# Optimization experiments

Measured on AMD Instinct MI355X. Metric: run time of the kernel, lower is better.

## Reference

```python
import jax, jax.numpy as jnp
import numpy as np
import math

B, T, C = 4, 2048, 1024
H = 16
D_FF = 4 * C


def new_gelu(x):
    # tanh-approx GELU, identical to the torch.jit.script version
    return 0.5 * x * (1.0 + jnp.tanh(math.sqrt(2.0 / math.pi) * (x + 0.044715 * x ** 3)))


def layernorm(x, g, b, eps=1e-5):
    mu = jnp.mean(x, axis=-1, keepdims=True)
    var = jnp.var(x, axis=-1, keepdims=True)
    return (x - mu) * jax.lax.rsqrt(var + eps) * g + b


def setup_inputs() -> dict:
    key = jax.random.key(0)
    ks = jax.random.split(key, 8)
    s = 0.02
    return {
        "x": jax.random.normal(ks[0], (B, T, C), dtype=jnp.float32),
        "ln1_g": jnp.ones((C,), jnp.float32),
        "ln1_b": jnp.zeros((C,), jnp.float32),
        "w_qkv": jax.random.normal(ks[1], (C, 3 * C), jnp.float32) * s,
        "b_qkv": jnp.zeros((3 * C,), jnp.float32),
        "w_attnproj": jax.random.normal(ks[2], (C, C), jnp.float32) * s,
        "b_attnproj": jnp.zeros((C,), jnp.float32),
        "ln2_g": jnp.ones((C,), jnp.float32),
        "ln2_b": jnp.zeros((C,), jnp.float32),
        "w_fc": jax.random.normal(ks[3], (C, D_FF), jnp.float32) * s,
        "b_fc": jnp.zeros((D_FF,), jnp.float32),
        "w_proj": jax.random.normal(ks[4], (D_FF, C), jnp.float32) * s,
        "b_proj": jnp.zeros((C,), jnp.float32),
    }


def _block(x, ln1_g, ln1_b, w_qkv, b_qkv, w_attnproj, b_attnproj,
           ln2_g, ln2_b, w_fc, b_fc, w_proj, b_proj):
    # --- self-attention (pre-LN, non-causal, dropout=0) ---
    h = layernorm(x, ln1_g, ln1_b)
    qkv = h @ w_qkv + b_qkv                       # [B,T,3C]
    q, k, v = jnp.split(qkv, 3, axis=-1)
    hd = C // H
    q = q.reshape(B, T, H, hd).transpose(0, 2, 1, 3)  # [B,H,T,hd]
    k = k.reshape(B, T, H, hd).transpose(0, 2, 1, 3)
    v = v.reshape(B, T, H, hd).transpose(0, 2, 1, 3)
    att = jnp.einsum('bhqd,bhkd->bhqk', q, k) * (1.0 / math.sqrt(hd))
    att = jax.nn.softmax(att, axis=-1)
    y = jnp.einsum('bhqk,bhkd->bhqd', att, v)
    y = y.transpose(0, 2, 1, 3).reshape(B, T, C)
    x = x + (y @ w_attnproj + b_attnproj)
    # --- MLP ---
    h = layernorm(x, ln2_g, ln2_b)
    h = new_gelu(h @ w_fc + b_fc)
    x = x + (h @ w_proj + b_proj)
    return x


def reference(x, ln1_g, ln1_b, w_qkv, b_qkv, w_attnproj, b_attnproj,
              ln2_g, ln2_b, w_fc, b_fc, w_proj, b_proj):
    return _block(x, ln1_g, ln1_b, w_qkv, b_qkv, w_attnproj, b_attnproj,
                  ln2_g, ln2_b, w_fc, b_fc, w_proj, b_proj)
```

## Files before the change

### kernel.cpp

```cpp
#include <hip/hip_runtime.h>


typedef __attribute__((ext_vector_type(8))) short short8;
typedef __attribute__((ext_vector_type(4))) float fx4;
typedef __attribute__((ext_vector_type(16))) float fx16;

__device__ __forceinline__ unsigned short f2bf(float f) {
    union { float f; unsigned u; } v; v.f = f;
    unsigned r = v.u + 0x7fffu + ((v.u >> 16) & 1u);
    return (unsigned short)(r >> 16);
}

__device__ __forceinline__ float fexp2(float x) {
#if __has_builtin(__builtin_amdgcn_exp2f)
    return __builtin_amdgcn_exp2f(x);
#else
    return __expf(x * 0.69314718055994531f);
#endif
}

__device__ __forceinline__ unsigned pack_trunc(float lo, float hi) {
    return __builtin_amdgcn_perm(__float_as_uint(hi), __float_as_uint(lo),
                                 0x07060302u);
}

__device__ __forceinline__ void ld_lds16(const void* g, void* l) {
    __builtin_amdgcn_global_load_lds(
        (const __attribute__((address_space(1))) unsigned int*)g,
        (__attribute__((address_space(3))) unsigned int*)l, 16, 0, 0);
}

__global__ __launch_bounds__(256) void transpose_all(
    const float* __restrict__ w0, unsigned short* __restrict__ o0,
    const float* __restrict__ w1, unsigned short* __restrict__ o1,
    const float* __restrict__ w2, unsigned short* __restrict__ o2,
    const float* __restrict__ w3, unsigned short* __restrict__ o3)
{
    __shared__ float tile[32][33];
    int b = blockIdx.x;
    const float* in; unsigned short* out; int R, Cn;
    if (b < 3072)      { in = w0; out = o0; R = 1024; Cn = 3072; }
    else if (b < 4096) { b -= 3072; in = w1; out = o1; R = 1024; Cn = 1024; }
    else if (b < 8192) { b -= 4096; in = w2; out = o2; R = 1024; Cn = 4096; }
    else               { b -= 8192; in = w3; out = o3; R = 4096; Cn = 1024; }
    int tilesX = Cn >> 5;
    int c0 = (b % tilesX) * 32, r0 = (b / tilesX) * 32;
    int tx = threadIdx.x, ty = threadIdx.y;
    for (int i = 0; i < 4; ++i)
        tile[ty + i * 8][tx] = in[(size_t)(r0 + ty + i * 8) * Cn + c0 + tx];
    __syncthreads();
    for (int i = 0; i < 4; ++i)
        out[(size_t)(c0 + ty + i * 8) * R + r0 + tx] = f2bf(tile[tx][ty + i * 8]);
}

__global__ __launch_bounds__(256) void layernorm_bf16(
    const float* __restrict__ x, const float* __restrict__ g,
    const float* __restrict__ bb, unsigned short* __restrict__ out)
{
    const int C = 1024;
    int row = blockIdx.x;
    const float* xr = x + (size_t)row * C;
    float4 v = ((const float4*)xr)[threadIdx.x];
    float s  = v.x + v.y + v.z + v.w;
    float ss = v.x * v.x + v.y * v.y + v.z * v.z + v.w * v.w;
    for (int off = 32; off >= 1; off >>= 1) {
        s  += __shfl_xor(s,  off);
        ss += __shfl_xor(ss, off);
    }
    __shared__ float sbuf[2][4];
    int wave = threadIdx.x >> 6;
    if ((threadIdx.x & 63) == 0) { sbuf[0][wave] = s; sbuf[1][wave] = ss; }
    __syncthreads();
    s  = sbuf[0][0] + sbuf[0][1] + sbuf[0][2] + sbuf[0][3];
    ss = sbuf[1][0] + sbuf[1][1] + sbuf[1][2] + sbuf[1][3];
    float mu   = s * (1.0f / C);
    float var  = ss * (1.0f / C) - mu * mu;
    float rstd = rsqrtf(var + 1e-5f);
    int i = threadIdx.x * 4;
    ushort4 o;
    o.x = f2bf((v.x - mu) * rstd * g[i + 0] + bb[i + 0]);
    o.y = f2bf((v.y - mu) * rstd * g[i + 1] + bb[i + 1]);
    o.z = f2bf((v.z - mu) * rstd * g[i + 2] + bb[i + 2]);
    o.w = f2bf((v.w - mu) * rstd * g[i + 3] + bb[i + 3]);
    ((ushort4*)(out + (size_t)row * C))[threadIdx.x] = o;
}

template <int EPI, bool SWAP>
__global__ __launch_bounds__(256) void gemm_bt(
    const unsigned short* __restrict__ A, const unsigned short* __restrict__ Bt,
    const float* __restrict__ bias, const float* __restrict__ resid,
    void* __restrict__ out0, void* __restrict__ out1, void* __restrict__ out2,
    int M, int N, int K)
{
    __shared__ unsigned short As[128 * 64];
    __shared__ unsigned short Bs[128 * 64];
    const int bm = (SWAP ? blockIdx.x : blockIdx.y) * 128;
    const int bn = (SWAP ? blockIdx.y : blockIdx.x) * 128;
    const int t = threadIdx.x, wave = t >> 6, lane = t & 63;
    const int wm = (wave >> 1) * 64, wn = (wave & 1) * 64;
    const int l32 = lane & 31, half = lane >> 5;

    int goff[4], loff[4];
    #pragma unroll
    for (int c = 0; c < 4; ++c) {
        int idx = t + c * 256;
        int row = idx >> 3, ps = idx & 7;
        int p = (ps - row) & 7;
        goff[c] = row * K + p * 8;
        loff[c] = idx * 8;
    }
    int aoffs[2][4], boffs[2][4];
    #pragma unroll
    for (int i = 0; i < 2; ++i)
        #pragma unroll
        for (int s = 0; s < 4; ++s) {
            int ra = wm + i * 32 + l32;
            int rb = wn + i * 32 + l32;
            aoffs[i][s] = ra * 64 + (((s * 2 + half + ra) & 7) << 3);
            boffs[i][s] = rb * 64 + (((s * 2 + half + rb) & 7) << 3);
        }

    const unsigned short* Ab = A + (size_t)bm * K;
    const unsigned short* Bb = Bt + (size_t)bn * K;

    fx16 acc[2][2];
    #pragma unroll
    for (int mi = 0; mi < 2; ++mi)
        #pragma unroll
        for (int ni = 0; ni < 2; ++ni)
            acc[mi][ni] = 0.0f;

    for (int it = 0, nit = K >> 6; it < nit; ++it) {
        #pragma unroll
        for (int c = 0; c < 4; ++c) {
            ld_lds16(Ab + goff[c], &As[loff[c]]);
            ld_lds16(Bb + goff[c], &Bs[loff[c]]);
        }
        Ab += 64; Bb += 64;
        __syncthreads();
        #pragma unroll
        for (int s = 0; s < 4; ++s) {
            short8 a0 = *(const short8*)&As[aoffs[0][s]];
            short8 a1 = *(const short8*)&As[aoffs[1][s]];
            short8 b0 = *(const short8*)&Bs[boffs[0][s]];
            short8 b1 = *(const short8*)&Bs[boffs[1][s]];
            acc[0][0] = __builtin_amdgcn_mfma_f32_32x32x16_bf16(a0, b0, acc[0][0], 0, 0, 0);
            acc[0][1] = __builtin_amdgcn_mfma_f32_32x32x16_bf16(a0, b1, acc[0][1], 0, 0, 0);
            acc[1][0] = __builtin_amdgcn_mfma_f32_32x32x16_bf16(a1, b0, acc[1][0], 0, 0, 0);
            acc[1][1] = __builtin_amdgcn_mfma_f32_32x32x16_bf16(a1, b1, acc[1][1], 0, 0, 0);
        }
        __syncthreads();
    }

    #pragma unroll
    for (int mi = 0; mi < 2; ++mi) {
        #pragma unroll
        for (int ni = 0; ni < 2; ++ni) {
            int col = bn + wn + ni * 32 + l32;
            float bcol = bias[col];
            #pragma unroll
            for (int reg = 0; reg < 16; ++reg) {
                int row = bm + wm + mi * 32 + (reg & 3) + 8 * (reg >> 2) + 4 * half;
                float v = acc[mi][ni][reg] + bcol;
                if constexpr (EPI == 0) {
                    int sec = col >> 10, cc = col & 1023;
                    int head = cc >> 6, d = cc & 63;
                    int batch = row >> 11, tt = row & 2047;
                    size_t bh = (size_t)(batch * 16 + head);
                    if (sec == 0)
                        ((unsigned short*)out0)[(bh * 2048 + tt) * 64 + d] =
                            f2bf(v * 0.18033688011112042f);
                    else if (sec == 1)
                        ((unsigned short*)out1)[(bh * 2048 + tt) * 64 + d] = f2bf(v);
                    else
                        ((unsigned short*)out2)[(bh * 64 + d) * 2048 + tt] = f2bf(v);
                } else if constexpr (EPI == 1) {
                    ((float*)out0)[(size_t)row * N + col] =
                        resid[(size_t)row * N + col] + v;
                } else {
                    float u2 = 1.5957691216057308f * (v + 0.044715f * v * v * v);
                    float gl = v * __builtin_amdgcn_rcpf(1.0f + __expf(-u2));
                    ((unsigned short*)out0)[(size_t)row * N + col] = f2bf(gl);
                }
            }
        }
    }
}

__global__ __launch_bounds__(256, 3) void flash_attn(
    const unsigned short* __restrict__ Q, const unsigned short* __restrict__ Kk,
    const unsigned short* __restrict__ Vt, unsigned short* __restrict__ Y)
{
    __shared__ unsigned short Ks[64 * 64];
    __shared__ unsigned short Vs[64 * 64];
    __shared__ unsigned short Ps[4][16 * 72];
    const int bh = blockIdx.y;
    const int batch = bh >> 4, head = bh & 15;
    const int t = threadIdx.x, w = t >> 6, lane = t & 63;
    const int lq = lane >> 4, lr = lane & 15;
    const int q0 = blockIdx.x * 128 + w * 32;
    const size_t base = (size_t)bh * 2048 * 64;

    short8 qf[2][2];
    #pragma unroll
    for (int qt = 0; qt < 2; ++qt)
        #pragma unroll
        for (int c = 0; c < 2; ++c)
            qf[qt][c] = *(const short8*)
                &Q[base + (size_t)(q0 + qt * 16 + lr) * 64 + c * 32 + lq * 8];

    int kg[2], vg[2], lo[2];
    #pragma unroll
    for (int c2 = 0; c2 < 2; ++c2) {
        int idx = t + c2 * 256;
        int row = idx >> 3, ps = idx & 7;
        int p = (ps - row) & 7;
        kg[c2] = row * 64 + p * 8;
        vg[c2] = row * 2048 + p * 8;
        lo[c2] = idx * 8;
    }
    int kvo[4][2];
    #pragma unroll
    for (int i = 0; i < 4; ++i)
        #pragma unroll
        for (int c = 0; c < 2; ++c) {
            int row = i * 16 + lr;
            kvo[i][c] = row * 64 + (((c * 4 + lq + row) & 7) << 3);
        }
    const unsigned short* Kb = Kk + base;
    const unsigned short* Vb = Vt + base;

    short8 ones;
    #pragma unroll
    for (int i = 0; i < 8; ++i) ones[i] = (short)0x3F80;

    fx4 lacc[2];
    fx4 o[2][4];
    #pragma unroll
    for (int qt = 0; qt < 2; ++qt) {
        lacc[qt] = 0.0f;
        #pragma unroll
        for (int dn = 0; dn < 4; ++dn) o[qt][dn] = 0.0f;
    }

    for (int kt = 0; kt < 32; ++kt) {
        __syncthreads();
        #pragma unroll
        for (int c2 = 0; c2 < 2; ++c2) {
            ld_lds16(Kb + kg[c2], &Ks[lo[c2]]);
            ld_lds16(Vb + vg[c2], &Vs[lo[c2]]);
        }
        Kb += 64 * 64; Vb += 64;
        __syncthreads();

        short8 kf[4][2], vf[4][2];
        #pragma unroll
        for (int kn = 0; kn < 4; ++kn)
            #pragma unroll
            for (int c = 0; c < 2; ++c)
                kf[kn][c] = *(const short8*)&Ks[kvo[kn][c]];
        #pragma unroll
        for (int dn = 0; dn < 4; ++dn)
            #pragma unroll
            for (int c = 0; c < 2; ++c)
                vf[dn][c] = *(const short8*)&Vs[kvo[dn][c]];

        #pragma unroll
        for (int qt = 0; qt < 2; ++qt) {
            #pragma unroll
            for (int kn = 0; kn < 4; ++kn) {
                fx4 s = 0.0f;
                s = __builtin_amdgcn_mfma_f32_16x16x32_bf16(
                    kf[kn][0], qf[qt][0], s, 0, 0, 0);
                s = __builtin_amdgcn_mfma_f32_16x16x32_bf16(
                    kf[kn][1], qf[qt][1], s, 0, 0, 0);
                float p0 = fexp2(s[0]);
                float p1 = fexp2(s[1]);
                float p2 = fexp2(s[2]);
                float p3 = fexp2(s[3]);
                uint2 pk;
                pk.x = pack_trunc(p0, p1);
                pk.y = pack_trunc(p2, p3);
                *(uint2*)&Ps[w][lr * 72 + kn * 16 + lq * 4] = pk;
            }
            short8 pf0 = *(const short8*)&Ps[w][lr * 72 + lq * 8];
            short8 pf1 = *(const short8*)&Ps[w][lr * 72 + 32 + lq * 8];
            lacc[qt] = __builtin_amdgcn_mfma_f32_16x16x32_bf16(
                ones, pf0, lacc[qt], 0, 0, 0);
            lacc[qt] = __builtin_amdgcn_mfma_f32_16x16x32_bf16(
                ones, pf1, lacc[qt], 0, 0, 0);
            #pragma unroll
            for (int dn = 0; dn < 4; ++dn) {
                o[qt][dn] = __builtin_amdgcn_mfma_f32_16x16x32_bf16(
                    vf[dn][0], pf0, o[qt][dn], 0, 0, 0);
                o[qt][dn] = __builtin_amdgcn_mfma_f32_16x16x32_bf16(
                    vf[dn][1], pf1, o[qt][dn], 0, 0, 0);
            }
        }
    }

    #pragma unroll
    for (int qt = 0; qt < 2; ++qt) {
        float inv = __builtin_amdgcn_rcpf(lacc[qt][0]);
        int qg = q0 + qt * 16 + lr;
        #pragma unroll
        for (int dn = 0; dn < 4; ++dn) {
            ushort4 ov;
            ov.x = f2bf(o[qt][dn][0] * inv);
            ov.y = f2bf(o[qt][dn][1] * inv);
            ov.z = f2bf(o[qt][dn][2] * inv);
            ov.w = f2bf(o[qt][dn][3] * inv);
            *(ushort4*)&Y[((size_t)(batch * 2048 + qg)) * 1024 +
                          head * 64 + dn * 16 + lq * 4] = ov;
        }
    }
}

extern "C" void kernel_launch(void* const* d_in, const int* in_sizes, int n_in,
                              void* d_out, int out_size, void* d_ws, size_t ws_size,
                              hipStream_t stream)
{
    const float* x      = (const float*)d_in[0];
    const float* ln1_g  = (const float*)d_in[1];
    const float* ln1_b  = (const float*)d_in[2];
    const float* w_qkv  = (const float*)d_in[3];
    const float* b_qkv  = (const float*)d_in[4];
    const float* w_ap   = (const float*)d_in[5];
    const float* b_ap   = (const float*)d_in[6];
    const float* ln2_g  = (const float*)d_in[7];
    const float* ln2_b  = (const float*)d_in[8];
    const float* w_fc   = (const float*)d_in[9];
    const float* b_fc   = (const float*)d_in[10];
    const float* w_proj = (const float*)d_in[11];
    const float* b_proj = (const float*)d_in[12];
    float* out = (float*)d_out;

    char* ws = (char*)d_ws;
    unsigned short* wT_qkv = (unsigned short*)(ws + 0);
    unsigned short* wT_ap  = (unsigned short*)(ws + 6291456);
    unsigned short* wT_fc  = (unsigned short*)(ws + 8388608);
    unsigned short* wT_pr  = (unsigned short*)(ws + 16777216);
    float*          x2     = (float*)(ws + 25165824);
    unsigned short* Abuf   = (unsigned short*)(ws + 58720256);
    unsigned short* Qb     = (unsigned short*)(ws + 75497472);
    unsigned short* Kb     = (unsigned short*)(ws + 75497472 + 16777216);
    unsigned short* Vtb    = (unsigned short*)(ws + 75497472 + 33554432);
    unsigned short* H3     = (unsigned short*)(ws + 75497472);

    transpose_all<<<12288, dim3(32, 8), 0, stream>>>(
        w_qkv, wT_qkv, w_ap, wT_ap, w_fc, wT_fc, w_proj, wT_pr);

    layernorm_bf16<<<8192, 256, 0, stream>>>(x, ln1_g, ln1_b, Abuf);
    gemm_bt<0, false><<<dim3(24, 64), 256, 0, stream>>>(
        Abuf, wT_qkv, b_qkv, nullptr, Qb, Kb, Vtb, 8192, 3072, 1024);
    flash_attn<<<dim3(16, 64), 256, 0, stream>>>(Qb, Kb, Vtb, Abuf);
    gemm_bt<1, true><<<dim3(64, 8), 256, 0, stream>>>(
        Abuf, wT_ap, b_ap, x, x2, nullptr, nullptr, 8192, 1024, 1024);
    layernorm_bf16<<<8192, 256, 0, stream>>>(x2, ln2_g, ln2_b, Abuf);
    gemm_bt<2, false><<<dim3(32, 64), 256, 0, stream>>>(
        Abuf, wT_fc, b_fc, nullptr, H3, nullptr, nullptr, 8192, 4096, 1024);
    gemm_bt<1, true><<<dim3(64, 8), 256, 0, stream>>>(
        H3, wT_pr, b_proj, x2, out, nullptr, nullptr, 8192, 1024, 4096);
}
```

Measured before the change: 510.3 us.

## Widen flash-attention query tile per wave and fuse weight prep with first layernorm

The flash attention kernel now gives each wave 64 query rows instead of 32, with 256 queries per block and half as many blocks. Each K/V tile loaded into LDS is reused across twice as many queries, and K fragments are read once per key block and shared across four query tiles. The weight-transpose kernel and the first layernorm are merged into one launch to save a kernel launch and its tail. The cost is more accumulator registers, a larger Ps shared buffer, and fewer blocks, which may lower occupancy under the existing launch_bounds(256,3).

```diff
diff --git a/kernel.cpp b/kernel.cpp
--- a/kernel.cpp
+++ b/kernel.cpp
@@ -30,27 +30,59 @@
         (__attribute__((address_space(3))) unsigned int*)l, 16, 0, 0);
 }
 
-__global__ __launch_bounds__(256) void transpose_all(
+__global__ __launch_bounds__(256) void prep_all(
     const float* __restrict__ w0, unsigned short* __restrict__ o0,
     const float* __restrict__ w1, unsigned short* __restrict__ o1,
     const float* __restrict__ w2, unsigned short* __restrict__ o2,
-    const float* __restrict__ w3, unsigned short* __restrict__ o3)
-{
-    __shared__ float tile[32][33];
+    const float* __restrict__ w3, unsigned short* __restrict__ o3,
+    const float* __restrict__ x, const float* __restrict__ g,
+    const float* __restrict__ bb, unsigned short* __restrict__ ln_out)
+{
     int b = blockIdx.x;
-    const float* in; unsigned short* out; int R, Cn;
-    if (b < 3072)      { in = w0; out = o0; R = 1024; Cn = 3072; }
-    else if (b < 4096) { b -= 3072; in = w1; out = o1; R = 1024; Cn = 1024; }
-    else if (b < 8192) { b -= 4096; in = w2; out = o2; R = 1024; Cn = 4096; }
-    else               { b -= 8192; in = w3; out = o3; R = 4096; Cn = 1024; }
-    int tilesX = Cn >> 5;
-    int c0 = (b % tilesX) * 32, r0 = (b / tilesX) * 32;
-    int tx = threadIdx.x, ty = threadIdx.y;
-    for (int i = 0; i < 4; ++i)
-        tile[ty + i * 8][tx] = in[(size_t)(r0 + ty + i * 8) * Cn + c0 + tx];
-    __syncthreads();
-    for (int i = 0; i < 4; ++i)
-        out[(size_t)(c0 + ty + i * 8) * R + r0 + tx] = f2bf(tile[tx][ty + i * 8]);
+    if (b < 12288) {
+        __shared__ float tile[32][33];
+        const float* in; unsigned short* out; int R, Cn;
+        if (b < 3072)      { in = w0; out = o0; R = 1024; Cn = 3072; }
+        else if (b < 4096) { b -= 3072; in = w1; out = o1; R = 1024; Cn = 1024; }
+        else if (b < 8192) { b -= 4096; in = w2; out = o2; R = 1024; Cn = 4096; }
+        else               { b -= 8192; in = w3; out = o3; R = 4096; Cn = 1024; }
+        int tilesX = Cn >> 5;
+        int c0 = (b % tilesX) * 32, r0 = (b / tilesX) * 32;
+        int tx = threadIdx.x & 31, ty = threadIdx.x >> 5;
+        for (int i = 0; i < 4; ++i)
+            tile[ty + i * 8][tx] = in[(size_t)(r0 + ty + i * 8) * Cn + c0 + tx];
+        __syncthreads();
+        for (int i = 0; i < 4; ++i)
+            out[(size_t)(c0 + ty + i * 8) * R + r0 + tx] =
+                f2bf(tile[tx][ty + i * 8]);
+    } else {
+        const int C = 1024;
+        int row = b - 12288;
+        const float* xr = x + (size_t)row * C;
+        float4 v = ((const float4*)xr)[threadIdx.x];
+        float s  = v.x + v.y + v.z + v.w;
+        float ss = v.x * v.x + v.y * v.y + v.z * v.z + v.w * v.w;
+        for (int off = 32; off >= 1; off >>= 1) {
+            s  += __shfl_xor(s,  off);
+            ss += __shfl_xor(ss, off);
+        }
+        __shared__ float sbuf[2][4];
+        int wave = threadIdx.x >> 6;
+        if ((threadIdx.x & 63) == 0) { sbuf[0][wave] = s; sbuf[1][wave] = ss; }
+        __syncthreads();
+        s  = sbuf[0][0] + sbuf[0][1] + sbuf[0][2] + sbuf[0][3];
+        ss = sbuf[1][0] + sbuf[1][1] + sbuf[1][2] + sbuf[1][3];
+        float mu   = s * (1.0f / C);
+        float var  = ss * (1.0f / C) - mu * mu;
+        float rstd = rsqrtf(var + 1e-5f);
+        int i = threadIdx.x * 4;
+        ushort4 o;
+        o.x = f2bf((v.x - mu) * rstd * g[i + 0] + bb[i + 0]);
+        o.y = f2bf((v.y - mu) * rstd * g[i + 1] + bb[i + 1]);
+        o.z = f2bf((v.z - mu) * rstd * g[i + 2] + bb[i + 2]);
+        o.w = f2bf((v.w - mu) * rstd * g[i + 3] + bb[i + 3]);
+        ((ushort4*)(ln_out + (size_t)row * C))[threadIdx.x] = o;
+    }
 }
 
 __global__ __launch_bounds__(256) void layernorm_bf16(
@@ -193,17 +225,17 @@
 {
     __shared__ unsigned short Ks[64 * 64];
     __shared__ unsigned short Vs[64 * 64];
-    __shared__ unsigned short Ps[4][16 * 72];
+    __shared__ unsigned short Ps[4][4][16 * 72];
     const int bh = blockIdx.y;
     const int batch = bh >> 4, head = bh & 15;
     const int t = threadIdx.x, w = t >> 6, lane = t & 63;
     const int lq = lane >> 4, lr = lane & 15;
-    const int q0 = blockIdx.x * 128 + w * 32;
+    const int q0 = blockIdx.x * 256 + w * 64;
     const size_t base = (size_t)bh * 2048 * 64;
 
-    short8 qf[2][2];
-    #pragma unroll
-    for (int qt = 0; qt < 2; ++qt)
+    short8 qf[4][2];
+    #pragma unroll
+    for (int qt = 0; qt < 4; ++qt)
         #pragma unroll
         for (int c = 0; c < 2; ++c)
             qf[qt][c] = *(const short8*)
@@ -234,10 +266,10 @@
     #pragma unroll
     for (int i = 0; i < 8; ++i) ones[i] = (short)0x3F80;
 
-    fx4 lacc[2];
-    fx4 o[2][4];
-    #pragma unroll
-    for (int qt = 0; qt < 2; ++qt) {
+    fx4 lacc[4];
+    fx4 o[4][4];
+    #pragma unroll
+    for (int qt = 0; qt < 4; ++qt) {
         lacc[qt] = 0.0f;
         #pragma unroll
         for (int dn = 0; dn < 4; ++dn) o[qt][dn] = 0.0f;
@@ -253,54 +285,40 @@
         Kb += 64 * 64; Vb += 64;
         __syncthreads();
 
-        short8 kf[4][2], vf[4][2];
-        #pragma unroll
-        for (int kn = 0; kn < 4; ++kn)
+        #pragma unroll
+        for (int kn = 0; kn < 4; ++kn) {
+            short8 kf0 = *(const short8*)&Ks[kvo[kn][0]];
+            short8 kf1 = *(const short8*)&Ks[kvo[kn][1]];
             #pragma unroll
-            for (int c = 0; c < 2; ++c)
-                kf[kn][c] = *(const short8*)&Ks[kvo[kn][c]];
-        #pragma unroll
-        for (int dn = 0; dn < 4; ++dn)
-            #pragma unroll
-            for (int c = 0; c < 2; ++c)
-                vf[dn][c] = *(const short8*)&Vs[kvo[dn][c]];
-
-        #pragma unroll
-        for (int qt = 0; qt < 2; ++qt) {
-            #pragma unroll
-            for (int kn = 0; kn < 4; ++kn) {
+            for (int qt = 0; qt < 4; ++qt) {
                 fx4 s = 0.0f;
-                s = __builtin_amdgcn_mfma_f32_16x16x32_bf16(
-                    kf[kn][0], qf[qt][0], s, 0, 0, 0);
-                s = __builtin_amdgcn_mfma_f32_16x16x32_bf16(
-                    kf[kn][1], qf[qt][1], s, 0, 0, 0);
-                float p0 = fexp2(s[0]);
-                float p1 = fexp2(s[1]);
-                float p2 = fexp2(s[2]);
-                float p3 = fexp2(s[3]);
+                s = __builtin_amdgcn_mfma_f32_16x16x32_bf16(kf0, qf[qt][0], s, 0, 0, 0);
+                s = __builtin_amdgcn_mfma_f32_16x16x32_bf16(kf1, qf[qt][1], s, 0, 0, 0);
                 uint2 pk;
-                pk.x = pack_trunc(p0, p1);
-                pk.y = pack_trunc(p2, p3);
-                *(uint2*)&Ps[w][lr * 72 + kn * 16 + lq * 4] = pk;
+                pk.x = pack_trunc(fexp2(s[0]), fexp2(s[1]));
+                pk.y = pack_trunc(fexp2(s[2]), fexp2(s[3]));
+                *(uint2*)&Ps[w][qt][lr * 72 + kn * 16 + lq * 4] = pk;
             }
-            short8 pf0 = *(const short8*)&Ps[w][lr * 72 + lq * 8];
-            short8 pf1 = *(const short8*)&Ps[w][lr * 72 + 32 + lq * 8];
-            lacc[qt] = __builtin_amdgcn_mfma_f32_16x16x32_bf16(
-                ones, pf0, lacc[qt], 0, 0, 0);
-            lacc[qt] = __builtin_amdgcn_mfma_f32_16x16x32_bf16(
-                ones, pf1, lacc[qt], 0, 0, 0);
+        }
+
+        #pragma unroll
+        for (int qt = 0; qt < 4; ++qt) {
+            short8 pf0 = *(const short8*)&Ps[w][qt][lr * 72 + lq * 8];
+            short8 pf1 = *(const short8*)&Ps[w][qt][lr * 72 + 32 + lq * 8];
+            lacc[qt] = __builtin_amdgcn_mfma_f32_16x16x32_bf16(ones, pf0, lacc[qt], 0, 0, 0);
+            lacc[qt] = __builtin_amdgcn_mfma_f32_16x16x32_bf16(ones, pf1, lacc[qt], 0, 0, 0);
             #pragma unroll
             for (int dn = 0; dn < 4; ++dn) {
-                o[qt][dn] = __builtin_amdgcn_mfma_f32_16x16x32_bf16(
-                    vf[dn][0], pf0, o[qt][dn], 0, 0, 0);
-                o[qt][dn] = __builtin_amdgcn_mfma_f32_16x16x32_bf16(
-                    vf[dn][1], pf1, o[qt][dn], 0, 0, 0);
+                short8 vf0 = *(const short8*)&Vs[kvo[dn][0]];
+                short8 vf1 = *(const short8*)&Vs[kvo[dn][1]];
+                o[qt][dn] = __builtin_amdgcn_mfma_f32_16x16x32_bf16(vf0, pf0, o[qt][dn], 0, 0, 0);
+                o[qt][dn] = __builtin_amdgcn_mfma_f32_16x16x32_bf16(vf1, pf1, o[qt][dn], 0, 0, 0);
             }
         }
     }
 
     #pragma unroll
-    for (int qt = 0; qt < 2; ++qt) {
+    for (int qt = 0; qt < 4; ++qt) {
         float inv = __builtin_amdgcn_rcpf(lacc[qt][0]);
         int qg = q0 + qt * 16 + lr;
         #pragma unroll
@@ -347,13 +365,12 @@
     unsigned short* Vtb    = (unsigned short*)(ws + 75497472 + 33554432);
     unsigned short* H3     = (unsigned short*)(ws + 75497472);
 
-    transpose_all<<<12288, dim3(32, 8), 0, stream>>>(
-        w_qkv, wT_qkv, w_ap, wT_ap, w_fc, wT_fc, w_proj, wT_pr);
-
-    layernorm_bf16<<<8192, 256, 0, stream>>>(x, ln1_g, ln1_b, Abuf);
+    prep_all<<<20480, 256, 0, stream>>>(w_qkv, wT_qkv, w_ap, wT_ap,
+                                        w_fc, wT_fc, w_proj, wT_pr,
+                                        x, ln1_g, ln1_b, Abuf);
     gemm_bt<0, false><<<dim3(24, 64), 256, 0, stream>>>(
         Abuf, wT_qkv, b_qkv, nullptr, Qb, Kb, Vtb, 8192, 3072, 1024);
-    flash_attn<<<dim3(16, 64), 256, 0, stream>>>(Qb, Kb, Vtb, Abuf);
+    flash_attn<<<dim3(8, 64), 256, 0, stream>>>(Qb, Kb, Vtb, Abuf);
     gemm_bt<1, true><<<dim3(64, 8), 256, 0, stream>>>(
         Abuf, wT_ap, b_ap, x, x2, nullptr, nullptr, 8192, 1024, 1024);
     layernorm_bf16<<<8192, 256, 0, stream>>>(x2, ln2_g, ln2_b, Abuf);
```

After: 534.0 us. 1.05x slower.
